# Kernel tuning notes

Hardware: AMD Instinct MI355X
Metric: run time of the kernel (lower is better)

The kernel has to match this reference:

```python
import jax, jax.numpy as jnp
import numpy as np

B, S, D, V, L = 8, 8192, 768, 64, 26  # batch, seq, hidden, symbol vocab, labels


def setup_inputs() -> dict:
    key = jax.random.key(0)
    k1, k2, k3 = jax.random.split(key, 3)
    hidden_states = jax.random.normal(k1, (B, S, D), dtype=jnp.float32)
    input_ids = jax.random.randint(k2, (B, S), 0, V, dtype=jnp.int32)
    W = jax.random.normal(k3, (L, D), dtype=jnp.float32) * 0.02
    b = jnp.zeros((L,), dtype=jnp.float32)
    return {"hidden_states": hidden_states, "W": W, "b": b, "input_ids": input_ids}


def reference(hidden_states, W, b, input_ids):
    # Per-batch, per-symbol mean pooling of hidden states, then linear classify.
    # Dense/padded equivalent of the torch per-symbol boolean-mask loop:
    # row (batch_b, symbol_v) = classifier(mean of hidden_states[b] where input_ids[b]==v),
    # masked to 0 for symbol 0 and for symbols absent in the sequence.
    Bv, Sv, Dv = hidden_states.shape
    seg = (input_ids + jnp.arange(Bv, dtype=input_ids.dtype)[:, None] * V).reshape(-1)
    flat_h = hidden_states.reshape(-1, Dv)
    sums = jax.ops.segment_sum(flat_h, seg, num_segments=Bv * V)            # [B*V, D]
    counts = jax.ops.segment_sum(
        jnp.ones((Bv * Sv,), dtype=hidden_states.dtype), seg, num_segments=Bv * V
    )                                                                        # [B*V]
    means = sums / jnp.maximum(counts, 1.0)[:, None]
    logits = means @ W.T + b                                                 # [B*V, L]
    present = (counts > 0) & ((jnp.arange(Bv * V) % V) > 0)                  # exclude symbol 0
    logits = jnp.where(present[:, None], logits, 0.0)
    return logits.reshape(Bv, V, -1)
```

## Files before the change

### kernel.cpp

```cpp
#include <hip/hip_runtime.h>

#define B_ 8
#define S_ 8192
#define D_ 768
#define V_ 64
#define L_ 26

typedef __attribute__((ext_vector_type(8))) short short8;
typedef __attribute__((ext_vector_type(4))) float floatx4;

#define TOKS 512
#define SLICES (S_ / TOKS)
#define NSL  48

__global__ __launch_bounds__(256, 2) void pool_mfma_kernel(
    const float* __restrict__ h, const int* __restrict__ ids,
    float* __restrict__ part, unsigned int* __restrict__ cntpart)
{
    __shared__ unsigned int cnt[V_];

    const int tid  = threadIdx.x;
    const int lane = tid & 63;
    const int wave = tid >> 6;
    const int nl   = lane & 15;
    const int quad = lane >> 4;

    const int b     = blockIdx.z;
    const int slice = blockIdx.x;
    const int k0    = slice * TOKS;
    const int n0    = blockIdx.y * (4 * NSL) + wave * NSL;

    const int*   idrow = ids + b * S_ + k0;
    const float* hrow  = h + ((size_t)b * S_ + k0) * D_ + n0;

    if (blockIdx.y == 0) {
        if (tid < V_) cnt[tid] = 0u;
        __syncthreads();
        if (tid < TOKS / 4) {
            const int4 q = ((const int4*)idrow)[tid];
            atomicAdd(&cnt[q.x], 1u); atomicAdd(&cnt[q.y], 1u);
            atomicAdd(&cnt[q.z], 1u); atomicAdd(&cnt[q.w], 1u);
        }
        __syncthreads();
        if (tid < V_) cntpart[(slice * B_ + b) * V_ + tid] = cnt[tid];
    }

    floatx4 acc[4][3];
    #pragma unroll
    for (int mt = 0; mt < 4; ++mt)
        #pragma unroll
        for (int nt = 0; nt < 3; ++nt) acc[mt][nt] = (floatx4)0.f;

    for (int ks = 0; ks < TOKS; ks += 32) {
        const int kb = ks + quad * 8;
        const int4* ip = (const int4*)(idrow + kb);
        const int4 i0 = ip[0], i1 = ip[1];
        const int idv[8] = {i0.x, i0.y, i0.z, i0.w, i1.x, i1.y, i1.z, i1.w};

        short8 afrag[4];
        #pragma unroll
        for (int mt = 0; mt < 4; ++mt) {
            const int m = mt * 16 + nl;
            #pragma unroll
            for (int j = 0; j < 8; ++j)
                afrag[mt][j] = (idv[j] == m) ? (short)0x3F80 : (short)0;
        }

        #pragma unroll
        for (int nt = 0; nt < 3; ++nt) {
            const float* bp = hrow + (size_t)kb * D_ + nt * 16 + nl;
            float f[8];
            #pragma unroll
            for (int j = 0; j < 8; ++j) f[j] = bp[(size_t)j * D_];
            short8 bhi, blo;
            #pragma unroll
            for (int j = 0; j < 8; ++j) {
                const unsigned u = __builtin_bit_cast(unsigned, f[j]);
                bhi[j] = (short)(u >> 16);
                const float hif = __builtin_bit_cast(float, u & 0xFFFF0000u);
                const float lof = f[j] - hif;
                blo[j] = (short)(__builtin_bit_cast(unsigned, lof) >> 16);
            }
            #pragma unroll
            for (int mt = 0; mt < 4; ++mt) {
                acc[mt][nt] = __builtin_amdgcn_mfma_f32_16x16x32_bf16(
                    afrag[mt], bhi, acc[mt][nt], 0, 0, 0);
                acc[mt][nt] = __builtin_amdgcn_mfma_f32_16x16x32_bf16(
                    afrag[mt], blo, acc[mt][nt], 0, 0, 0);
            }
        }
    }

    float* pbase = part + ((size_t)(slice * B_ + b) * V_) * D_;
    #pragma unroll
    for (int mt = 0; mt < 4; ++mt)
        #pragma unroll
        for (int nt = 0; nt < 3; ++nt)
            #pragma unroll
            for (int r = 0; r < 4; ++r) {
                const int v = mt * 16 + quad * 4 + r;
                const int d = n0 + nt * 16 + nl;
                pbase[(size_t)v * D_ + d] = acc[mt][nt][r];
            }
}

__global__ __launch_bounds__(256) void reduce_finalize_kernel(
    const float* __restrict__ part, const unsigned int* __restrict__ cntpart,
    const float* __restrict__ Wm, const float* __restrict__ bias,
    float* __restrict__ out)
{
    __shared__ float mean[D_];
    __shared__ unsigned int scnt;

    const int tid = threadIdx.x;
    const int bv  = blockIdx.x;
    const int b   = bv >> 6;
    const int v   = bv & (V_ - 1);

    if (tid == 0) scnt = 0u;
    __syncthreads();
    if (tid < SLICES)
        atomicAdd(&scnt, cntpart[(tid * B_ + b) * V_ + v]);

    float s[3];
    #pragma unroll
    for (int j = 0; j < 3; ++j) {
        const int d = tid + j * 256;
        float a = 0.f;
        #pragma unroll
        for (int sl = 0; sl < SLICES; ++sl)
            a += part[((size_t)(sl * B_ + b) * V_ + v) * D_ + d];
        s[j] = a;
    }
    __syncthreads();
    const unsigned int c = scnt;
    const float inv = 1.f / (float)(c > 1u ? c : 1u);
    #pragma unroll
    for (int j = 0; j < 3; ++j) mean[tid + j * 256] = s[j] * inv;
    __syncthreads();

    const bool present = (c > 0u) && (v > 0);
    const int lane = tid & 63;
    const int wave = tid >> 6;
    for (int l = wave; l < L_; l += 4) {
        const float* wrow = Wm + l * D_;
        float p = 0.f;
        #pragma unroll
        for (int j = 0; j < 12; ++j) {
            const int d = lane + 64 * j;
            p += mean[d] * wrow[d];
        }
        #pragma unroll
        for (int off = 32; off > 0; off >>= 1) p += __shfl_down(p, off);
        if (lane == 0) out[bv * L_ + l] = present ? (p + bias[l]) : 0.f;
    }
}

extern "C" void kernel_launch(void* const* d_in, const int* in_sizes, int n_in,
                              void* d_out, int out_size, void* d_ws, size_t ws_size,
                              hipStream_t stream) {
    const float* h    = (const float*)d_in[0];
    const float* Wm   = (const float*)d_in[1];
    const float* bias = (const float*)d_in[2];
    const int*   ids  = (const int*)d_in[3];
    float* out = (float*)d_out;

    float* part = (float*)d_ws;
    unsigned int* cntpart =
        (unsigned int*)(part + (size_t)SLICES * B_ * V_ * D_);

    dim3 grid1(SLICES, D_ / (4 * NSL), B_);
    pool_mfma_kernel<<<grid1, 256, 0, stream>>>(h, ids, part, cntpart);

    reduce_finalize_kernel<<<B_ * V_, 256, 0, stream>>>(
        part, cntpart, Wm, bias, out);
}
```

Measured before the change: 297.5 us.

## Double-buffer hidden-state loads and shrink per-wave column tile in pooling kernel

The pooling kernel now software-pipelines its token loop, loading ids and hidden values for the next 32-token step into registers while the current step runs its MFMAs. Each wave now covers 32 columns instead of 48, so the grid has 6 column blocks instead of 4. Launch bounds go up to 3 blocks per SM to raise occupancy and hide global-load latency. The cost is more register pressure from the double buffers and more blocks re-reading the id rows.

```diff
diff --git a/kernel.cpp b/kernel.cpp
--- a/kernel.cpp
+++ b/kernel.cpp
@@ -11,9 +11,11 @@
 
 #define TOKS 512
 #define SLICES (S_ / TOKS)
-#define NSL  48
+#define WNSL 32
+#define BCOLS 128
+#define KSTEPS (TOKS / 32)
 
-__global__ __launch_bounds__(256, 2) void pool_mfma_kernel(
+__global__ __launch_bounds__(256, 3) void pool_mfma_kernel(
     const float* __restrict__ h, const int* __restrict__ ids,
     float* __restrict__ part, unsigned int* __restrict__ cntpart)
 {
@@ -28,7 +30,7 @@
     const int b     = blockIdx.z;
     const int slice = blockIdx.x;
     const int k0    = slice * TOKS;
-    const int n0    = blockIdx.y * (4 * NSL) + wave * NSL;
+    const int n0    = blockIdx.y * BCOLS + wave * WNSL;
 
     const int*   idrow = ids + b * S_ + k0;
     const float* hrow  = h + ((size_t)b * S_ + k0) * D_ + n0;
@@ -45,18 +47,30 @@
         if (tid < V_) cntpart[(slice * B_ + b) * V_ + tid] = cnt[tid];
     }
 
-    floatx4 acc[4][3];
+    floatx4 acc[4][2];
     #pragma unroll
     for (int mt = 0; mt < 4; ++mt)
         #pragma unroll
-        for (int nt = 0; nt < 3; ++nt) acc[mt][nt] = (floatx4)0.f;
+        for (int nt = 0; nt < 2; ++nt) acc[mt][nt] = (floatx4)0.f;
 
-    for (int ks = 0; ks < TOKS; ks += 32) {
-        const int kb = ks + quad * 8;
+    int4  idA0, idA1, idB0, idB1;
+    float fA[2][8], fB[2][8];
+
+    auto load_step = [&](int m, int4& i0, int4& i1, float f[2][8]) {
+        const int kb = m * 32 + quad * 8;
         const int4* ip = (const int4*)(idrow + kb);
-        const int4 i0 = ip[0], i1 = ip[1];
+        i0 = ip[0]; i1 = ip[1];
+        const float* bp = hrow + (size_t)kb * D_ + nl;
+        #pragma unroll
+        for (int t = 0; t < 2; ++t)
+            #pragma unroll
+            for (int j = 0; j < 8; ++j)
+                f[t][j] = bp[(size_t)j * D_ + t * 16];
+    };
+
+    auto compute_step = [&](const int4& i0, const int4& i1,
+                            const float f[2][8]) {
         const int idv[8] = {i0.x, i0.y, i0.z, i0.w, i1.x, i1.y, i1.z, i1.w};
-
         short8 afrag[4];
         #pragma unroll
         for (int mt = 0; mt < 4; ++mt) {
@@ -65,37 +79,40 @@
             for (int j = 0; j < 8; ++j)
                 afrag[mt][j] = (idv[j] == m) ? (short)0x3F80 : (short)0;
         }
-
         #pragma unroll
-        for (int nt = 0; nt < 3; ++nt) {
-            const float* bp = hrow + (size_t)kb * D_ + nt * 16 + nl;
-            float f[8];
-            #pragma unroll
-            for (int j = 0; j < 8; ++j) f[j] = bp[(size_t)j * D_];
+        for (int t = 0; t < 2; ++t) {
             short8 bhi, blo;
             #pragma unroll
             for (int j = 0; j < 8; ++j) {
-                const unsigned u = __builtin_bit_cast(unsigned, f[j]);
+                const unsigned u = __builtin_bit_cast(unsigned, f[t][j]);
                 bhi[j] = (short)(u >> 16);
                 const float hif = __builtin_bit_cast(float, u & 0xFFFF0000u);
-                const float lof = f[j] - hif;
+                const float lof = f[t][j] - hif;
                 blo[j] = (short)(__builtin_bit_cast(unsigned, lof) >> 16);
             }
             #pragma unroll
             for (int mt = 0; mt < 4; ++mt) {
-                acc[mt][nt] = __builtin_amdgcn_mfma_f32_16x16x32_bf16(
-                    afrag[mt], bhi, acc[mt][nt], 0, 0, 0);
-                acc[mt][nt] = __builtin_amdgcn_mfma_f32_16x16x32_bf16(
-                    afrag[mt], blo, acc[mt][nt], 0, 0, 0);
+                acc[mt][t] = __builtin_amdgcn_mfma_f32_16x16x32_bf16(
+                    afrag[mt], bhi, acc[mt][t], 0, 0, 0);
+                acc[mt][t] = __builtin_amdgcn_mfma_f32_16x16x32_bf16(
+                    afrag[mt], blo, acc[mt][t], 0, 0, 0);
             }
         }
+    };
+
+    load_step(0, idA0, idA1, fA);
+    for (int ks = 0; ks < KSTEPS; ks += 2) {
+        load_step(ks + 1, idB0, idB1, fB);
+        compute_step(idA0, idA1, fA);
+        if (ks + 2 < KSTEPS) load_step(ks + 2, idA0, idA1, fA);
+        compute_step(idB0, idB1, fB);
     }
 
     float* pbase = part + ((size_t)(slice * B_ + b) * V_) * D_;
     #pragma unroll
     for (int mt = 0; mt < 4; ++mt)
         #pragma unroll
-        for (int nt = 0; nt < 3; ++nt)
+        for (int nt = 0; nt < 2; ++nt)
             #pragma unroll
             for (int r = 0; r < 4; ++r) {
                 const int v = mt * 16 + quad * 4 + r;
@@ -169,7 +186,7 @@
     unsigned int* cntpart =
         (unsigned int*)(part + (size_t)SLICES * B_ * V_ * D_);
 
-    dim3 grid1(SLICES, D_ / (4 * NSL), B_);
+    dim3 grid1(SLICES, D_ / BCOLS, B_);
     pool_mfma_kernel<<<grid1, 256, 0, stream>>>(h, ids, part, cntpart);
 
     reduce_finalize_kernel<<<B_ * V_, 256, 0, stream>>>(
```

Result: no change. 299.7 us (+0.8%).

## Stage hidden-state tiles in LDS via global_load_lds and use 32x32 MFMA

Applied to the files above, without the earlier changes.

The pooling kernel now copies 64x128 tiles of hidden states straight into shared memory with global_load_lds, replacing the strided per-lane scalar global loads. It switches from 16x16x32 to 32x32x16 bf16 MFMA with a 32-column-per-wave tile, and raises the occupancy hint to 4 blocks per CU. The goal is coalesced, wider global traffic and fewer MFMA issues per byte. The cost is an extra barrier per tile with no double buffering, so load latency is not overlapped within a block.

```diff
diff --git a/kernel.cpp b/kernel.cpp
--- a/kernel.cpp
+++ b/kernel.cpp
@@ -6,32 +6,35 @@
 #define V_ 64
 #define L_ 26
 
-typedef __attribute__((ext_vector_type(8))) short short8;
-typedef __attribute__((ext_vector_type(4))) float floatx4;
+typedef __attribute__((ext_vector_type(8)))  short short8;
+typedef __attribute__((ext_vector_type(16))) float floatx16;
 
 #define TOKS 512
 #define SLICES (S_ / TOKS)
-#define NSL  48
+#define BCOLS 128
+#define KT 64
+#define NTILES (TOKS / KT)
 
-__global__ __launch_bounds__(256, 2) void pool_mfma_kernel(
+__global__ __launch_bounds__(256, 4) void pool_mfma_kernel(
     const float* __restrict__ h, const int* __restrict__ ids,
     float* __restrict__ part, unsigned int* __restrict__ cntpart)
 {
+    __shared__ float tile[KT * BCOLS];
     __shared__ unsigned int cnt[V_];
 
-    const int tid  = threadIdx.x;
-    const int lane = tid & 63;
-    const int wave = tid >> 6;
-    const int nl   = lane & 15;
-    const int quad = lane >> 4;
+    const int tid   = threadIdx.x;
+    const int lane  = tid & 63;
+    const int wave  = tid >> 6;
+    const int nn    = lane & 31;
+    const int khalf = lane >> 5;
 
     const int b     = blockIdx.z;
     const int slice = blockIdx.x;
     const int k0    = slice * TOKS;
-    const int n0    = blockIdx.y * (4 * NSL) + wave * NSL;
+    const int n0blk = blockIdx.y * BCOLS;
+    const int nw    = wave * 32;
 
-    const int*   idrow = ids + b * S_ + k0;
-    const float* hrow  = h + ((size_t)b * S_ + k0) * D_ + n0;
+    const int* idrow = ids + b * S_ + k0;
 
     if (blockIdx.y == 0) {
         if (tid < V_) cnt[tid] = 0u;
@@ -45,33 +48,48 @@
         if (tid < V_) cntpart[(slice * B_ + b) * V_ + tid] = cnt[tid];
     }
 
-    floatx4 acc[4][3];
-    #pragma unroll
-    for (int mt = 0; mt < 4; ++mt)
+    floatx16 acc[2];
+    acc[0] = (floatx16)0.f;
+    acc[1] = (floatx16)0.f;
+
+    const char* gblk = (const char*)(h + ((size_t)(b * S_ + k0) * D_ + n0blk));
+    const size_t lane_off = (size_t)(lane >> 5) * (D_ * 4) + (size_t)(lane & 31) * 16;
+    const int r0 = wave * 16;
+
+    for (int t = 0; t < NTILES; ++t) {
+        const char* gtile = gblk + (size_t)(t * KT) * (D_ * 4);
         #pragma unroll
-        for (int nt = 0; nt < 3; ++nt) acc[mt][nt] = (floatx4)0.f;
+        for (int i = 0; i < 8; ++i) {
+            const int r = r0 + 2 * i;
+            const char* gp = gtile + (size_t)r * (D_ * 4) + lane_off;
+            __builtin_amdgcn_global_load_lds(
+                (const __attribute__((address_space(1))) unsigned int*)gp,
+                (__attribute__((address_space(3))) unsigned int*)&tile[r * BCOLS],
+                16, 0, 0);
+        }
+        __syncthreads();
 
-    for (int ks = 0; ks < TOKS; ks += 32) {
-        const int kb = ks + quad * 8;
-        const int4* ip = (const int4*)(idrow + kb);
-        const int4 i0 = ip[0], i1 = ip[1];
-        const int idv[8] = {i0.x, i0.y, i0.z, i0.w, i1.x, i1.y, i1.z, i1.w};
+        #pragma unroll
+        for (int ss = 0; ss < KT / 16; ++ss) {
+            const int kb = ss * 16 + khalf * 8;
+            const int4 i0 = *(const int4*)(idrow + t * KT + kb);
+            const int4 i1 = *(const int4*)(idrow + t * KT + kb + 4);
+            const int idv[8] = {i0.x, i0.y, i0.z, i0.w, i1.x, i1.y, i1.z, i1.w};
 
-        short8 afrag[4];
-        #pragma unroll
-        for (int mt = 0; mt < 4; ++mt) {
-            const int m = mt * 16 + nl;
+            short8 af[2];
+            #pragma unroll
+            for (int mt = 0; mt < 2; ++mt) {
+                const int m = mt * 32 + nn;
+                #pragma unroll
+                for (int j = 0; j < 8; ++j)
+                    af[mt][j] = (idv[j] == m) ? (short)0x3F80 : (short)0;
+            }
+
+            float f[8];
             #pragma unroll
             for (int j = 0; j < 8; ++j)
-                afrag[mt][j] = (idv[j] == m) ? (short)0x3F80 : (short)0;
-        }
+                f[j] = tile[(kb + j) * BCOLS + nw + nn];
 
-        #pragma unroll
-        for (int nt = 0; nt < 3; ++nt) {
-            const float* bp = hrow + (size_t)kb * D_ + nt * 16 + nl;
-            float f[8];
-            #pragma unroll
-            for (int j = 0; j < 8; ++j) f[j] = bp[(size_t)j * D_];
             short8 bhi, blo;
             #pragma unroll
             for (int j = 0; j < 8; ++j) {
@@ -81,27 +99,27 @@
                 const float lof = f[j] - hif;
                 blo[j] = (short)(__builtin_bit_cast(unsigned, lof) >> 16);
             }
+
             #pragma unroll
-            for (int mt = 0; mt < 4; ++mt) {
-                acc[mt][nt] = __builtin_amdgcn_mfma_f32_16x16x32_bf16(
-                    afrag[mt], bhi, acc[mt][nt], 0, 0, 0);
-                acc[mt][nt] = __builtin_amdgcn_mfma_f32_16x16x32_bf16(
-                    afrag[mt], blo, acc[mt][nt], 0, 0, 0);
+            for (int mt = 0; mt < 2; ++mt) {
+                acc[mt] = __builtin_amdgcn_mfma_f32_32x32x16_bf16(
+                    af[mt], bhi, acc[mt], 0, 0, 0);
+                acc[mt] = __builtin_amdgcn_mfma_f32_32x32x16_bf16(
+                    af[mt], blo, acc[mt], 0, 0, 0);
             }
         }
+        __syncthreads();
     }
 
-    float* pbase = part + ((size_t)(slice * B_ + b) * V_) * D_;
+    float* pbase = part + (size_t)(slice * B_ + b) * V_ * D_;
+    const int d = n0blk + nw + nn;
     #pragma unroll
-    for (int mt = 0; mt < 4; ++mt)
+    for (int mt = 0; mt < 2; ++mt)
         #pragma unroll
-        for (int nt = 0; nt < 3; ++nt)
-            #pragma unroll
-            for (int r = 0; r < 4; ++r) {
-                const int v = mt * 16 + quad * 4 + r;
-                const int d = n0 + nt * 16 + nl;
-                pbase[(size_t)v * D_ + d] = acc[mt][nt][r];
-            }
+        for (int r = 0; r < 16; ++r) {
+            const int v = mt * 32 + (r & 3) + 8 * (r >> 2) + 4 * khalf;
+            pbase[(size_t)v * D_ + d] = acc[mt][r];
+        }
 }
 
 __global__ __launch_bounds__(256) void reduce_finalize_kernel(
@@ -169,7 +187,7 @@
     unsigned int* cntpart =
         (unsigned int*)(part + (size_t)SLICES * B_ * V_ * D_);
 
-    dim3 grid1(SLICES, D_ / (4 * NSL), B_);
+    dim3 grid1(SLICES, D_ / BCOLS, B_);
     pool_mfma_kernel<<<grid1, 256, 0, stream>>>(h, ids, part, cntpart);
 
     reduce_finalize_kernel<<<B_ * V_, 256, 0, stream>>>(
```

Measured after the change: 299.1 us. No clear change (+0.5%).
